# Kernel tuning notes

Measured on AMD Instinct MI355X. Metric: run time of the kernel, lower is better.

## Reference

```python
import jax, jax.numpy as jnp
import numpy as np

N, D, H, Y = 2048, 768, 12, 64


def setup_inputs() -> dict:
    key = jax.random.key(0)
    kg, kq, kk = jax.random.split(key, 3)
    g = jax.random.normal(kg, (N, D), dtype=jnp.float32)
    Wq = jax.random.normal(kq, (H, Y, D), dtype=jnp.float32)
    Wk = jax.random.normal(kk, (H, Y, D), dtype=jnp.float32)
    return {"g": g, "Wq": Wq, "Wk": Wk}


def reference(g, Wq, Wk):
    # g: [N, D]; Wq, Wk: [H, Y, D]
    beta = 1.0 / jnp.sqrt(jnp.asarray(Y, dtype=g.dtype))
    K = jnp.einsum('kd,hzd->khz', g, Wk)          # [N, H, Y]
    Q = jnp.einsum('qd,hzd->qhz', g, Wq)          # [N, H, Y]
    scores = beta * jnp.einsum('qhz,khz->hqk', Q, K)  # [H, N, N]
    A = jax.nn.logsumexp(scores, axis=-1)         # [H, N]
    return (-1.0 / beta) * A.sum()
```

## Files before the change

kernel.cpp:

```cpp
#include <hip/hip_runtime.h>
#include <hip/hip_bf16.h>

#define NN 2048
#define DD 768
#define HH 12
#define HW 1536
#define SPLITS 4
#define KPW (NN/SPLITS)
#define NCH (KPW/64)

typedef __attribute__((ext_vector_type(8))) short bf16x8;
typedef __attribute__((ext_vector_type(4))) float f32x4;

__device__ __forceinline__ float exp2g(float x) { return __builtin_amdgcn_exp2f(x); }
__device__ __forceinline__ float log2g(float x) { return __builtin_amdgcn_logf(x); }

#define QSCALE 0.18033688011112042f

__device__ __forceinline__ unsigned short bfbits(float x) {
  __hip_bfloat16 h = __float2bfloat16(x);
  return *reinterpret_cast<unsigned short*>(&h);
}

__device__ __forceinline__ void cvt_store(__hip_bfloat16* dst, float4 a, float4 b, float sc) {
  union { uint4 v; unsigned short s[8]; } u;
  u.s[0] = bfbits(a.x * sc); u.s[1] = bfbits(a.y * sc);
  u.s[2] = bfbits(a.z * sc); u.s[3] = bfbits(a.w * sc);
  u.s[4] = bfbits(b.x * sc); u.s[5] = bfbits(b.y * sc);
  u.s[6] = bfbits(b.z * sc); u.s[7] = bfbits(b.w * sc);
  *reinterpret_cast<uint4*>(dst) = u.v;
}

#define LDP 72
__global__ __launch_bounds__(256) void proj_kernel(
    const float* __restrict__ g, const float* __restrict__ Wq,
    const float* __restrict__ Wk, __hip_bfloat16* __restrict__ QK,
    float* __restrict__ out) {
  __shared__ __align__(16) __hip_bfloat16 As[2][64 * LDP];
  __shared__ __align__(16) __hip_bfloat16 Bs[2][64 * LDP];
  if (blockIdx.x == 0 && blockIdx.y == 0 && threadIdx.x == 0) out[0] = 0.0f;
  const int t = threadIdx.x;
  const int wave = t >> 6, lane = t & 63;
  const int lr = lane & 15, lg = lane >> 4;
  const int wm = wave & 1, wn = wave >> 1;
  const int bm = blockIdx.x, bn = blockIdx.y;
  const int r0 = t >> 3, s0 = (t & 7) * 8;
  const int r1 = (t + 256) >> 3;

  const float bscale = (bn < HH) ? QSCALE : 1.0f;
  const float* wsrc = (bn < HH) ? Wq : Wk;
  const int wrow = (bn < HH) ? bn * 64 : (bn - HH) * 64;

  const float* ga0 = g + (bm * 64 + r0) * DD + s0;
  const float* ga1 = g + (bm * 64 + r1) * DD + s0;
  const float* gb0 = wsrc + (wrow + r0) * DD + s0;
  const float* gb1 = wsrc + (wrow + r1) * DD + s0;

  f32x4 acc[2][2] = {};

  {
    float4 a0 = *reinterpret_cast<const float4*>(ga0);
    float4 a0h = *reinterpret_cast<const float4*>(ga0 + 4);
    float4 a1 = *reinterpret_cast<const float4*>(ga1);
    float4 a1h = *reinterpret_cast<const float4*>(ga1 + 4);
    float4 b0 = *reinterpret_cast<const float4*>(gb0);
    float4 b0h = *reinterpret_cast<const float4*>(gb0 + 4);
    float4 b1 = *reinterpret_cast<const float4*>(gb1);
    float4 b1h = *reinterpret_cast<const float4*>(gb1 + 4);
    cvt_store(&As[0][r0 * LDP + s0], a0, a0h, 1.0f);
    cvt_store(&As[0][r1 * LDP + s0], a1, a1h, 1.0f);
    cvt_store(&Bs[0][r0 * LDP + s0], b0, b0h, bscale);
    cvt_store(&Bs[0][r1 * LDP + s0], b1, b1h, bscale);
  }
  __syncthreads();

  for (int it = 0; it < 12; ++it) {
    const int cur = it & 1;
    float4 na0, na0h, na1, na1h, nb0, nb0h, nb1, nb1h;
    if (it < 11) {
      const int kt = (it + 1) * 64;
      na0 = *reinterpret_cast<const float4*>(ga0 + kt);
      na0h = *reinterpret_cast<const float4*>(ga0 + kt + 4);
      na1 = *reinterpret_cast<const float4*>(ga1 + kt);
      na1h = *reinterpret_cast<const float4*>(ga1 + kt + 4);
      nb0 = *reinterpret_cast<const float4*>(gb0 + kt);
      nb0h = *reinterpret_cast<const float4*>(gb0 + kt + 4);
      nb1 = *reinterpret_cast<const float4*>(gb1 + kt);
      nb1h = *reinterpret_cast<const float4*>(gb1 + kt + 4);
    }
#pragma unroll
    for (int ks = 0; ks < 2; ++ks) {
      bf16x8 a[2], b[2];
#pragma unroll
      for (int mt = 0; mt < 2; ++mt)
        a[mt] = *reinterpret_cast<const bf16x8*>(&As[cur][(wm * 32 + mt * 16 + lr) * LDP + ks * 32 + lg * 8]);
#pragma unroll
      for (int nt = 0; nt < 2; ++nt)
        b[nt] = *reinterpret_cast<const bf16x8*>(&Bs[cur][(wn * 32 + nt * 16 + lr) * LDP + ks * 32 + lg * 8]);
#pragma unroll
      for (int mt = 0; mt < 2; ++mt)
#pragma unroll
        for (int nt = 0; nt < 2; ++nt)
          acc[mt][nt] = __builtin_amdgcn_mfma_f32_16x16x32_bf16(a[mt], b[nt], acc[mt][nt], 0, 0, 0);
    }
    if (it < 11) {
      cvt_store(&As[cur ^ 1][r0 * LDP + s0], na0, na0h, 1.0f);
      cvt_store(&As[cur ^ 1][r1 * LDP + s0], na1, na1h, 1.0f);
      cvt_store(&Bs[cur ^ 1][r0 * LDP + s0], nb0, nb0h, bscale);
      cvt_store(&Bs[cur ^ 1][r1 * LDP + s0], nb1, nb1h, bscale);
      __syncthreads();
    }
  }
#pragma unroll
  for (int mt = 0; mt < 2; ++mt) {
    int row = bm * 64 + wm * 32 + mt * 16 + lg * 4;
#pragma unroll
    for (int nt = 0; nt < 2; ++nt) {
      int col = bn * 64 + wn * 32 + nt * 16 + lr;
#pragma unroll
      for (int r = 0; r < 4; ++r)
        QK[(row + r) * HW + col] = __float2bfloat16(acc[mt][nt][r]);
    }
  }
}

__global__ __launch_bounds__(256, 3) void attn_kernel(
    const __hip_bfloat16* __restrict__ QK, float2* __restrict__ part) {
  const int t = threadIdx.x;
  const int wave = t >> 6, lane = t & 63;
  const int lr = lane & 15, lg = lane >> 4;
  const int q0 = blockIdx.x * 128, h = blockIdx.y, sp = blockIdx.z;
  const int k0 = sp * KPW;

  bf16x8 aq[2][2];
#pragma unroll
  for (int mt = 0; mt < 2; ++mt)
#pragma unroll
    for (int z = 0; z < 2; ++z)
      aq[mt][z] = *reinterpret_cast<const bf16x8*>(
          QK + (q0 + wave * 32 + mt * 16 + lr) * HW + h * 64 + z * 32 + lg * 8);

  const __hip_bfloat16* kb = QK + (k0 + lr) * HW + DD + h * 64 + lg * 8;

  float m[2][4], l[2][4];
#pragma unroll
  for (int mt = 0; mt < 2; ++mt)
#pragma unroll
    for (int r = 0; r < 4; ++r) { m[mt][r] = -3.0e38f; l[mt][r] = 0.0f; }

  bf16x8 b[4][2];
#pragma unroll
  for (int nt = 0; nt < 4; ++nt)
#pragma unroll
    for (int z = 0; z < 2; ++z)
      b[nt][z] = *reinterpret_cast<const bf16x8*>(kb + nt * 16 * HW + z * 32);

#pragma unroll
  for (int ci = 0; ci < NCH; ++ci) {
    bf16x8 nb[4][2];
    if (ci < NCH - 1) {
      const __hip_bfloat16* nk = kb + (ci + 1) * 64 * HW;
#pragma unroll
      for (int nt = 0; nt < 4; ++nt)
#pragma unroll
        for (int z = 0; z < 2; ++z)
          nb[nt][z] = *reinterpret_cast<const bf16x8*>(nk + nt * 16 * HW + z * 32);
    }

    f32x4 s[2][4] = {};
#pragma unroll
    for (int mt = 0; mt < 2; ++mt)
#pragma unroll
      for (int nt = 0; nt < 4; ++nt)
#pragma unroll
        for (int z = 0; z < 2; ++z)
          s[mt][nt] = __builtin_amdgcn_mfma_f32_16x16x32_bf16(aq[mt][z], b[nt][z], s[mt][nt], 0, 0, 0);

#pragma unroll
    for (int mt = 0; mt < 2; ++mt)
#pragma unroll
      for (int r = 0; r < 4; ++r) {
        float v0 = s[mt][0][r], v1 = s[mt][1][r], v2 = s[mt][2][r], v3 = s[mt][3][r];
        float cm = fmaxf(fmaxf(v0, v1), fmaxf(v2, v3));
        float mn = fmaxf(m[mt][r], cm);
        float p = exp2g(v0 - mn) + exp2g(v1 - mn) +
                  exp2g(v2 - mn) + exp2g(v3 - mn);
        l[mt][r] = l[mt][r] * exp2g(m[mt][r] - mn) + p;
        m[mt][r] = mn;
      }

    if (ci < NCH - 1) {
#pragma unroll
      for (int nt = 0; nt < 4; ++nt)
#pragma unroll
        for (int z = 0; z < 2; ++z)
          b[nt][z] = nb[nt][z];
    }
  }

#pragma unroll
  for (int msk = 1; msk <= 8; msk <<= 1) {
#pragma unroll
    for (int mt = 0; mt < 2; ++mt)
#pragma unroll
      for (int r = 0; r < 4; ++r) {
        float mo = __shfl_xor(m[mt][r], msk);
        float lo = __shfl_xor(l[mt][r], msk);
        float mn = fmaxf(m[mt][r], mo);
        l[mt][r] = l[mt][r] * exp2g(m[mt][r] - mn) + lo * exp2g(mo - mn);
        m[mt][r] = mn;
      }
  }
  if (lr == 0) {
#pragma unroll
    for (int mt = 0; mt < 2; ++mt)
#pragma unroll
      for (int r = 0; r < 4; ++r) {
        int q = q0 + wave * 32 + mt * 16 + lg * 4 + r;
        part[(sp * HH + h) * NN + q] = make_float2(m[mt][r], l[mt][r]);
      }
  }
}

__global__ __launch_bounds__(1024) void reduce_kernel(
    const float2* __restrict__ part, float* __restrict__ out) {
  const int t = threadIdx.x;
  const int row = blockIdx.x * 1024 + t;
  float2 p0 = part[row];
  float2 p1 = part[24576 + row];
  float2 p2 = part[49152 + row];
  float2 p3 = part[73728 + row];
  float mm = fmaxf(fmaxf(p0.x, p1.x), fmaxf(p2.x, p3.x));
  float ll = p0.y * exp2g(p0.x - mm) + p1.y * exp2g(p1.x - mm) +
             p2.y * exp2g(p2.x - mm) + p3.y * exp2g(p3.x - mm);
  float lse = mm + log2g(ll);
#pragma unroll
  for (int msk = 1; msk <= 32; msk <<= 1)
    lse += __shfl_xor(lse, msk);
  __shared__ float wsum[16];
  if ((t & 63) == 0) wsum[t >> 6] = lse;
  __syncthreads();
  if (t == 0) {
    float s = 0.0f;
#pragma unroll
    for (int i = 0; i < 16; ++i) s += wsum[i];
    atomicAdd(out, -5.545177444479562f * s);
  }
}

extern "C" void kernel_launch(void* const* d_in, const int* in_sizes, int n_in,
                              void* d_out, int out_size, void* d_ws, size_t ws_size,
                              hipStream_t stream) {
  const float* g  = (const float*)d_in[0];
  const float* Wq = (const float*)d_in[1];
  const float* Wk = (const float*)d_in[2];
  float* out = (float*)d_out;

  __hip_bfloat16* QK = (__hip_bfloat16*)d_ws;
  float2* part = (float2*)((char*)d_ws + (size_t)NN * HW * 2);

  proj_kernel<<<dim3(32, 24), 256, 0, stream>>>(g, Wq, Wk, QK, out);
  attn_kernel<<<dim3(16, HH, SPLITS), 256, 0, stream>>>(QK, part);
  reduce_kernel<<<24, 1024, 0, stream>>>(part, out);
}
```

Before: 106.8 us.

## Stage K tiles through double-buffered LDS in attention kernel

Each block now loads each 64-row K chunk cooperatively into a padded, double-buffered shared-memory tile and reads MFMA operands from LDS. Before, every wave loaded the same K fragments directly from global memory. This cuts redundant global loads across the four waves. In exchange it adds a block barrier per chunk, removes the full unroll of the chunk loop, and drops the occupancy hint of 3 in launch_bounds.

```diff
diff --git a/kernel.cpp b/kernel.cpp
--- a/kernel.cpp
+++ b/kernel.cpp
@@ -124,13 +124,18 @@
   }
 }
 
-__global__ __launch_bounds__(256, 3) void attn_kernel(
+#define LDA 72
+__global__ __launch_bounds__(256) void attn_kernel(
     const __hip_bfloat16* __restrict__ QK, float2* __restrict__ part) {
+  __shared__ __align__(16) __hip_bfloat16 Ks[2][64 * LDA];
   const int t = threadIdx.x;
   const int wave = t >> 6, lane = t & 63;
   const int lr = lane & 15, lg = lane >> 4;
   const int q0 = blockIdx.x * 128, h = blockIdx.y, sp = blockIdx.z;
   const int k0 = sp * KPW;
+  const int r0 = t >> 3, s0 = (t & 7) * 8;
+  const int r1 = (t + 256) >> 3, s1 = s0;
+  const int colK = DD + h * 64;
 
   bf16x8 aq[2][2];
 #pragma unroll
@@ -140,7 +145,11 @@
       aq[mt][z] = *reinterpret_cast<const bf16x8*>(
           QK + (q0 + wave * 32 + mt * 16 + lr) * HW + h * 64 + z * 32 + lg * 8);
 
-  const __hip_bfloat16* kb = QK + (k0 + lr) * HW + DD + h * 64 + lg * 8;
+  *reinterpret_cast<uint4*>(&Ks[0][r0 * LDA + s0]) =
+      *reinterpret_cast<const uint4*>(QK + (k0 + r0) * HW + colK + s0);
+  *reinterpret_cast<uint4*>(&Ks[0][r1 * LDA + s1]) =
+      *reinterpret_cast<const uint4*>(QK + (k0 + r1) * HW + colK + s1);
+  __syncthreads();
 
   float m[2][4], l[2][4];
 #pragma unroll
@@ -148,24 +157,20 @@
 #pragma unroll
     for (int r = 0; r < 4; ++r) { m[mt][r] = -3.0e38f; l[mt][r] = 0.0f; }
 
-  bf16x8 b[4][2];
-#pragma unroll
-  for (int nt = 0; nt < 4; ++nt)
-#pragma unroll
-    for (int z = 0; z < 2; ++z)
-      b[nt][z] = *reinterpret_cast<const bf16x8*>(kb + nt * 16 * HW + z * 32);
-
-#pragma unroll
   for (int ci = 0; ci < NCH; ++ci) {
-    bf16x8 nb[4][2];
+    const int cur = ci & 1;
+    uint4 n0, n1;
     if (ci < NCH - 1) {
-      const __hip_bfloat16* nk = kb + (ci + 1) * 64 * HW;
-#pragma unroll
-      for (int nt = 0; nt < 4; ++nt)
-#pragma unroll
-        for (int z = 0; z < 2; ++z)
-          nb[nt][z] = *reinterpret_cast<const bf16x8*>(nk + nt * 16 * HW + z * 32);
-    }
+      int kc = k0 + (ci + 1) * 64;
+      n0 = *reinterpret_cast<const uint4*>(QK + (kc + r0) * HW + colK + s0);
+      n1 = *reinterpret_cast<const uint4*>(QK + (kc + r1) * HW + colK + s1);
+    }
+    bf16x8 b[4][2];
+#pragma unroll
+    for (int nt = 0; nt < 4; ++nt)
+#pragma unroll
+      for (int z = 0; z < 2; ++z)
+        b[nt][z] = *reinterpret_cast<const bf16x8*>(&Ks[cur][(nt * 16 + lr) * LDA + z * 32 + lg * 8]);
 
     f32x4 s[2][4] = {};
 #pragma unroll
@@ -188,16 +193,12 @@
         l[mt][r] = l[mt][r] * exp2g(m[mt][r] - mn) + p;
         m[mt][r] = mn;
       }
-
     if (ci < NCH - 1) {
-#pragma unroll
-      for (int nt = 0; nt < 4; ++nt)
-#pragma unroll
-        for (int z = 0; z < 2; ++z)
-          b[nt][z] = nb[nt][z];
-    }
-  }
-
+      *reinterpret_cast<uint4*>(&Ks[cur ^ 1][r0 * LDA + s0]) = n0;
+      *reinterpret_cast<uint4*>(&Ks[cur ^ 1][r1 * LDA + s1]) = n1;
+      __syncthreads();
+    }
+  }
 #pragma unroll
   for (int msk = 1; msk <= 8; msk <<= 1) {
 #pragma unroll
```

Measured after the change: 96.89 us. 1.1x faster.
